# Kernel tuning notes

Measured on AMD Instinct MI355X. Metric: run time of the kernel, lower is better.

Reference implementation:

```python
import jax, jax.numpy as jnp
import numpy as np

TEMPERATURE = 0.07
EPS = 1e-8  # torch CosineSimilarity eps


def setup_inputs() -> dict:
    key = jax.random.key(0)
    k1, k2, k3 = jax.random.split(key, 3)
    N, D = 8192, 512
    features = jax.random.normal(k1, (N, D), dtype=jnp.float32)
    positive_mask = jax.random.randint(k2, (N, N), 0, 2, dtype=jnp.int32)
    negative_mask = jax.random.randint(k3, (N, N), 0, 2, dtype=jnp.int32)
    return {"features": features, "positive_mask": positive_mask, "negative_mask": negative_mask}


def reference(features, positive_mask, negative_mask):
    N = positive_mask.shape[0]
    self_contrast = 1.0 - jnp.eye(N, dtype=features.dtype)  # zero diagonal
    pos = positive_mask.astype(features.dtype) * self_contrast  # [N, N]
    neg = negative_mask.astype(features.dtype) * self_contrast  # [N, N]

    # cosine similarity via normalized matmul (same math as broadcasted CosineSimilarity)
    norm = jnp.maximum(jnp.linalg.norm(features, axis=1, keepdims=True), EPS)
    fn = features / norm  # [N, D]
    sim = jnp.matmul(fn, fn.T) / TEMPERATURE  # [N, N]

    logits_max = jax.lax.stop_gradient(jnp.max(sim, axis=1, keepdims=True))
    e = jnp.exp(sim - logits_max)  # [N, N]

    positives = e * pos
    log_neg_sum = jnp.log(jnp.sum(e * neg, axis=1, keepdims=True))  # [N, 1]
    log_prob = positives - log_neg_sum  # [N, N] (faithful to source: exp-masked, not log)

    cardinal = jnp.sum(pos, axis=1)
    cardinal = jnp.where(cardinal == 0, 1.0, cardinal)
    log_prob_sum = jnp.sum(log_prob * pos, axis=1)
    loss = -log_prob_sum / cardinal
    return jnp.mean(loss)
```

## Files before the change

kernel.cpp:

```cpp
#include <hip/hip_runtime.h>
#include <hip/hip_bf16.h>
#include <math.h>

#define NN 8192
#define DD 512
#define INV_T 14.285714285714286f

typedef __attribute__((ext_vector_type(8))) short s16x8;
typedef __attribute__((ext_vector_type(4))) float f32x4;

__device__ __forceinline__ unsigned short f32_to_bf16(float f) {
  unsigned int u = __float_as_uint(f);
  u += 0x7FFFu + ((u >> 16) & 1u);
  return (unsigned short)(u >> 16);
}

__device__ __forceinline__ void async16(const void* g, void* l) {
  __builtin_amdgcn_global_load_lds((__attribute__((address_space(1))) void*)(void*)g,
                                   (__attribute__((address_space(3))) void*)l,
                                   16, 0, 0);
}

__global__ __launch_bounds__(256) void normalize_kernel(const float* __restrict__ f,
                                                        unsigned short* __restrict__ fnb,
                                                        float* __restrict__ acc) {
  if (blockIdx.x < 96) acc[blockIdx.x * 256 + threadIdx.x] = 0.f;

  const int wave = threadIdx.x >> 6;
  const int lane = threadIdx.x & 63;
  const int row  = blockIdx.x * 4 + wave;
  const float* src = f + (size_t)row * DD + lane * 8;
  float4 v0 = *(const float4*)src;
  float4 v1 = *(const float4*)(src + 4);
  float ss = v0.x*v0.x + v0.y*v0.y + v0.z*v0.z + v0.w*v0.w
           + v1.x*v1.x + v1.y*v1.y + v1.z*v1.z + v1.w*v1.w;
  #pragma unroll
  for (int o = 32; o; o >>= 1) ss += __shfl_xor(ss, o);
  const float r = 1.0f / fmaxf(sqrtf(ss), 1e-8f);
  ushort4 a, b;
  a.x = f32_to_bf16(v0.x * r); a.y = f32_to_bf16(v0.y * r);
  a.z = f32_to_bf16(v0.z * r); a.w = f32_to_bf16(v0.w * r);
  b.x = f32_to_bf16(v1.x * r); b.y = f32_to_bf16(v1.y * r);
  b.z = f32_to_bf16(v1.z * r); b.w = f32_to_bf16(v1.w * r);
  unsigned short* dst = fnb + (size_t)row * DD + lane * 8;
  *(ushort4*)dst = a;
  *(ushort4*)(dst + 4) = b;
}

__global__ __launch_bounds__(256, 3) void fused_kernel(const unsigned short* __restrict__ fnb,
                                                       const int* __restrict__ posm,
                                                       const int* __restrict__ negm,
                                                       float* __restrict__ Spos,
                                                       float* __restrict__ Sneg,
                                                       float* __restrict__ Pcnt) {
  const int bid = blockIdx.x;
  int bi = (int)(64.5 - sqrt(64.5 * 64.5 - 2.0 * (double)bid));
  while (64 * bi - bi * (bi - 1) / 2 > bid) --bi;
  while (64 * (bi + 1) - (bi + 1) * bi / 2 <= bid) ++bi;
  const int bj = bi + (bid - (64 * bi - bi * (bi - 1) / 2));
  const int I = bi * 128;
  const int J = bj * 128;
  const bool offdiag = (bi != bj);

  const int tid  = threadIdx.x;
  const int wave = tid >> 6;
  const int lane = tid & 63;
  const int wm = wave >> 1;
  const int wn = wave & 1;
  const int q   = lane >> 4;
  const int c16 = lane & 15;

  __shared__ alignas(16) unsigned short lA[128 * 32];
  __shared__ alignas(16) unsigned short lB[128 * 32];
  __shared__ float sacc[2][128][3];
  __shared__ unsigned long long pk[4][128][2];
  for (int t = tid; t < 2 * 128 * 3; t += 256) ((float*)sacc)[t] = 0.f;

  f32x4 acc[4][4];
  const f32x4 z4 = {0.f, 0.f, 0.f, 0.f};
  #pragma unroll
  for (int mt = 0; mt < 4; ++mt)
    #pragma unroll
    for (int nt = 0; nt < 4; ++nt) acc[mt][nt] = z4;

  for (int kk = 0; kk < DD / 32; ++kk) {
    const int k0 = kk * 32;
    #pragma unroll
    for (int c = 0; c < 2; ++c) {
      const int fidx = tid + c * 256;
      const int L    = fidx >> 2;
      const int p    = fidx & 3;
      const int csrc = (p ^ ((L >> 1) & 3)) & 3;
      async16(fnb + (size_t)(I + L) * DD + k0 + csrc * 8, (char*)lA + fidx * 16);
      const int gB = 4 * (L & 31) + (L >> 5);
      async16(fnb + (size_t)(J + gB) * DD + k0 + csrc * 8, (char*)lB + fidx * 16);
    }
    __syncthreads();

    const int kd    = kk & 3;
    const int slice = kk >> 2;
    const bool mact = (kd < 2) || offdiag;
    int mv[16];
    if (mact) {
      const int rbase = (kd & 2) ? J : I;
      const int cbase = (kd & 2) ? I : J;
      const int* __restrict__ mp = (kd & 1) ? negm : posm;
      const int trow0 = slice * 32 + wave * 8;
      #pragma unroll
      for (int j = 0; j < 16; ++j) {
        const int trow = trow0 + (j >> 1);
        mv[j] = mp[(size_t)(rbase + trow) * NN + cbase + (j & 1) * 64 + lane];
      }
    }

    s16x8 aF[4], bF[4];
    #pragma unroll
    for (int t = 0; t < 4; ++t) {
      const int arow = wm * 64 + t * 16 + c16;
      const int apos = (q ^ ((arow >> 1) & 3)) & 3;
      aF[t] = *(const s16x8*)((const char*)lA + arow * 64 + apos * 16);
      const int Lb = (wn * 16 + c16) | (t << 5);
      const int bpos = (q ^ ((Lb >> 1) & 3)) & 3;
      bF[t] = *(const s16x8*)((const char*)lB + Lb * 64 + bpos * 16);
    }
    #pragma unroll
    for (int mt = 0; mt < 4; ++mt)
      #pragma unroll
      for (int nt = 0; nt < 4; ++nt)
        acc[mt][nt] = __builtin_amdgcn_mfma_f32_16x16x32_bf16(aF[mt], bF[nt], acc[mt][nt], 0, 0, 0);

    if (mact) {
      const int trow0 = slice * 32 + wave * 8;
      #pragma unroll
      for (int j = 0; j < 16; ++j) {
        const unsigned long long b = __ballot(mv[j] != 0);
        if (lane == j) pk[kd][trow0 + (j >> 1)][j & 1] = b;
      }
    }
    __syncthreads();
  }

  #pragma unroll
  for (int mt = 0; mt < 4; ++mt)
    #pragma unroll
    for (int nt = 0; nt < 4; ++nt)
      #pragma unroll
      for (int r = 0; r < 4; ++r)
        acc[mt][nt][r] = __expf(acc[mt][nt][r] * INV_T - INV_T);

  const bool hasdiag = (bi == bj) && (wm == wn);
  const int cb = wn * 64 + 4 * c16;
  const int half = c16 >> 3;
  const int bsh  = 4 * (c16 & 7);

  #pragma unroll
  for (int mt = 0; mt < 4; ++mt) {
    const int rl = wm * 64 + mt * 16 + q * 4;
    #pragma unroll
    for (int r = 0; r < 4; ++r) {
      const int row = rl + r;
      const uint2 pw = *(const uint2*)&pk[0][row][wn];
      const uint2 nw = *(const uint2*)&pk[1][row][wn];
      const unsigned int p32 = half ? pw.y : pw.x;
      const unsigned int n32 = half ? nw.y : nw.x;
      float dsp = 0.f, dsn = 0.f, dpc = 0.f;
      #pragma unroll
      for (int nt = 0; nt < 4; ++nt) {
        float pf = (float)((p32 >> (bsh + nt)) & 1u);
        float nf = (float)((n32 >> (bsh + nt)) & 1u);
        if (hasdiag && (row == cb + nt)) { pf = 0.f; nf = 0.f; }
        const float e = acc[mt][nt][r];
        dsp = fmaf(e, pf, dsp);
        dsn = fmaf(e, nf, dsn);
        dpc += pf;
      }
      #pragma unroll
      for (int o = 1; o <= 8; o <<= 1) {
        dsp += __shfl_xor(dsp, o);
        dsn += __shfl_xor(dsn, o);
        dpc += __shfl_xor(dpc, o);
      }
      if (c16 == 0) {
        atomicAdd(&sacc[0][row][0], dsp);
        atomicAdd(&sacc[0][row][1], dsn);
        atomicAdd(&sacc[0][row][2], dpc);
      }
    }
  }

  if (offdiag) {
    #pragma unroll
    for (int nt = 0; nt < 4; ++nt) {
      const int trl = cb + nt;
      const uint2 pw = *(const uint2*)&pk[2][trl][wm];
      const uint2 nw = *(const uint2*)&pk[3][trl][wm];
      float ts = 0.f, tn = 0.f, tp = 0.f;
      #pragma unroll
      for (int mt = 0; mt < 4; ++mt) {
        const unsigned int p32 = (mt < 2) ? pw.x : pw.y;
        const unsigned int n32 = (mt < 2) ? nw.x : nw.y;
        #pragma unroll
        for (int r = 0; r < 4; ++r) {
          const int bit = (mt & 1) * 16 + q * 4 + r;
          const float pf = (float)((p32 >> bit) & 1u);
          const float nf = (float)((n32 >> bit) & 1u);
          const float e = acc[mt][nt][r];
          ts = fmaf(e, pf, ts);
          tn = fmaf(e, nf, tn);
          tp += pf;
        }
      }
      ts += __shfl_xor(ts, 16); ts += __shfl_xor(ts, 32);
      tn += __shfl_xor(tn, 16); tn += __shfl_xor(tn, 32);
      tp += __shfl_xor(tp, 16); tp += __shfl_xor(tp, 32);
      if (q == 0) {
        atomicAdd(&sacc[1][trl][0], ts);
        atomicAdd(&sacc[1][trl][1], tn);
        atomicAdd(&sacc[1][trl][2], tp);
      }
    }
  }

  __syncthreads();

  const int r = tid & 127;
  if (tid < 128) {
    atomicAdd(&Spos[I + r], sacc[0][r][0]);
    atomicAdd(&Sneg[I + r], sacc[0][r][1]);
    atomicAdd(&Pcnt[I + r], sacc[0][r][2]);
  } else if (offdiag) {
    atomicAdd(&Spos[J + r], sacc[1][r][0]);
    atomicAdd(&Sneg[J + r], sacc[1][r][1]);
    atomicAdd(&Pcnt[J + r], sacc[1][r][2]);
  }
}

__global__ __launch_bounds__(256) void finalize_kernel(const float* __restrict__ Spos,
                                                       const float* __restrict__ Sneg,
                                                       const float* __restrict__ Pcnt,
                                                       float* __restrict__ out) {
  float local = 0.f;
  for (int i = threadIdx.x; i < NN; i += 256) {
    const float sp = Spos[i], sn = Sneg[i], pc = Pcnt[i];
    const float card = (pc == 0.f) ? 1.f : pc;
    local += (logf(sn) * pc - sp) / card;
  }
  #pragma unroll
  for (int o = 32; o; o >>= 1) local += __shfl_xor(local, o);
  __shared__ float red[4];
  if ((threadIdx.x & 63) == 0) red[threadIdx.x >> 6] = local;
  __syncthreads();
  if (threadIdx.x == 0)
    out[0] = (red[0] + red[1] + red[2] + red[3]) * (1.0f / (float)NN);
}

extern "C" void kernel_launch(void* const* d_in, const int* in_sizes, int n_in,
                              void* d_out, int out_size, void* d_ws, size_t ws_size,
                              hipStream_t stream) {
  const float* feat = (const float*)d_in[0];
  const int* posm   = (const int*)d_in[1];
  const int* negm   = (const int*)d_in[2];
  float* out = (float*)d_out;

  char* ws = (char*)d_ws;
  unsigned short* fnb = (unsigned short*)ws;
  float* Spos = (float*)(ws + (size_t)8 * 1024 * 1024);
  float* Sneg = Spos + NN;
  float* Pcnt = Sneg + NN;

  normalize_kernel<<<NN / 4, 256, 0, stream>>>(feat, fnb, Spos);
  fused_kernel<<<2080, 256, 0, stream>>>(fnb, posm, negm, Spos, Sneg, Pcnt);
  finalize_kernel<<<1, 256, 0, stream>>>(Spos, Sneg, Pcnt, out);
}
```

Before: 568.6 us.

## Pre-pack int masks into bitmasks in prep kernel, load bits in fused kernel

Mask bit-packing moves out of the GEMM main loop into the normalization kernel, which streams both int32 masks once with nontemporal loads and writes 64-bit ballot words to workspace. The fused kernel then loads the packed words for its tile pair into shared memory up front, so its K loop no longer issues scattered int32 mask loads that compete with the MFMA work. In exchange the prep kernel now carries the full mask read, and there is an extra write and read of the small packed arrays. The pk shared array is padded to avoid bank conflicts.

```diff
diff --git a/kernel.cpp b/kernel.cpp
--- a/kernel.cpp
+++ b/kernel.cpp
@@ -21,14 +21,19 @@
                                    16, 0, 0);
 }
 
-__global__ __launch_bounds__(256) void normalize_kernel(const float* __restrict__ f,
-                                                        unsigned short* __restrict__ fnb,
-                                                        float* __restrict__ acc) {
+__global__ __launch_bounds__(256) void prep_kernel(const float* __restrict__ f,
+                                                   const int* __restrict__ posm,
+                                                   const int* __restrict__ negm,
+                                                   unsigned short* __restrict__ fnb,
+                                                   unsigned long long* __restrict__ pkp,
+                                                   unsigned long long* __restrict__ pkn,
+                                                   float* __restrict__ acc) {
   if (blockIdx.x < 96) acc[blockIdx.x * 256 + threadIdx.x] = 0.f;
 
   const int wave = threadIdx.x >> 6;
   const int lane = threadIdx.x & 63;
   const int row  = blockIdx.x * 4 + wave;
+
   const float* src = f + (size_t)row * DD + lane * 8;
   float4 v0 = *(const float4*)src;
   float4 v1 = *(const float4*)(src + 4);
@@ -45,11 +50,35 @@
   unsigned short* dst = fnb + (size_t)row * DD + lane * 8;
   *(ushort4*)dst = a;
   *(ushort4*)(dst + 4) = b;
+
+  const int* __restrict__ prow = posm + (size_t)row * NN;
+  const int* __restrict__ nrow = negm + (size_t)row * NN;
+  #pragma unroll 2
+  for (int w = 0; w < 128; w += 4) {
+    unsigned long long pb[4], nb[4];
+    int pv[4], nv[4];
+    #pragma unroll
+    for (int u = 0; u < 4; ++u) {
+      pv[u] = __builtin_nontemporal_load(prow + (w + u) * 64 + lane);
+      nv[u] = __builtin_nontemporal_load(nrow + (w + u) * 64 + lane);
+    }
+    #pragma unroll
+    for (int u = 0; u < 4; ++u) {
+      pb[u] = __ballot(pv[u] != 0);
+      nb[u] = __ballot(nv[u] != 0);
+    }
+    unsigned long long rp = pb[0], rn = nb[0];
+    rp = ((lane & 3) == 1) ? pb[1] : rp;  rn = ((lane & 3) == 1) ? nb[1] : rn;
+    rp = ((lane & 3) == 2) ? pb[2] : rp;  rn = ((lane & 3) == 2) ? nb[2] : rn;
+    rp = ((lane & 3) == 3) ? pb[3] : rp;  rn = ((lane & 3) == 3) ? nb[3] : rn;
+    if (lane < 4)               pkp[(size_t)row * 128 + w + lane]       = rp;
+    else if (lane < 8)          pkn[(size_t)row * 128 + w + (lane - 4)] = rn;
+  }
 }
 
 __global__ __launch_bounds__(256, 3) void fused_kernel(const unsigned short* __restrict__ fnb,
-                                                       const int* __restrict__ posm,
-                                                       const int* __restrict__ negm,
+                                                       const unsigned long long* __restrict__ pkp,
+                                                       const unsigned long long* __restrict__ pkn,
                                                        float* __restrict__ Spos,
                                                        float* __restrict__ Sneg,
                                                        float* __restrict__ Pcnt) {
@@ -73,8 +102,21 @@
   __shared__ alignas(16) unsigned short lA[128 * 32];
   __shared__ alignas(16) unsigned short lB[128 * 32];
   __shared__ float sacc[2][128][3];
-  __shared__ unsigned long long pk[4][128][2];
+  __shared__ unsigned long long pk[4][128][3];
   for (int t = tid; t < 2 * 128 * 3; t += 256) ((float*)sacc)[t] = 0.f;
+
+  #pragma unroll
+  for (int p = 0; p < 2; ++p) {
+    const int idx  = tid + p * 256;
+    const int kind = idx >> 7;
+    const int row  = idx & 127;
+    const int rb   = (kind & 2) ? J : I;
+    const int cb6  = (kind & 2) ? (I >> 6) : (J >> 6);
+    const unsigned long long* __restrict__ m = (kind & 1) ? pkn : pkp;
+    const ulonglong2 v = *(const ulonglong2*)(m + (size_t)(rb + row) * 128 + cb6);
+    pk[kind][row][0] = v.x;
+    pk[kind][row][1] = v.y;
+  }
 
   f32x4 acc[4][4];
   const f32x4 z4 = {0.f, 0.f, 0.f, 0.f};
@@ -97,22 +139,6 @@
     }
     __syncthreads();
 
-    const int kd    = kk & 3;
-    const int slice = kk >> 2;
-    const bool mact = (kd < 2) || offdiag;
-    int mv[16];
-    if (mact) {
-      const int rbase = (kd & 2) ? J : I;
-      const int cbase = (kd & 2) ? I : J;
-      const int* __restrict__ mp = (kd & 1) ? negm : posm;
-      const int trow0 = slice * 32 + wave * 8;
-      #pragma unroll
-      for (int j = 0; j < 16; ++j) {
-        const int trow = trow0 + (j >> 1);
-        mv[j] = mp[(size_t)(rbase + trow) * NN + cbase + (j & 1) * 64 + lane];
-      }
-    }
-
     s16x8 aF[4], bF[4];
     #pragma unroll
     for (int t = 0; t < 4; ++t) {
@@ -128,15 +154,6 @@
       #pragma unroll
       for (int nt = 0; nt < 4; ++nt)
         acc[mt][nt] = __builtin_amdgcn_mfma_f32_16x16x32_bf16(aF[mt], bF[nt], acc[mt][nt], 0, 0, 0);
-
-    if (mact) {
-      const int trow0 = slice * 32 + wave * 8;
-      #pragma unroll
-      for (int j = 0; j < 16; ++j) {
-        const unsigned long long b = __ballot(mv[j] != 0);
-        if (lane == j) pk[kd][trow0 + (j >> 1)][j & 1] = b;
-      }
-    }
     __syncthreads();
   }
 
@@ -263,12 +280,14 @@
   float* out = (float*)d_out;
 
   char* ws = (char*)d_ws;
-  unsigned short* fnb = (unsigned short*)ws;
-  float* Spos = (float*)(ws + (size_t)8 * 1024 * 1024);
+  unsigned short* fnb      = (unsigned short*)ws;
+  unsigned long long* pkp  = (unsigned long long*)(ws + (size_t) 8*1024*1024);
+  unsigned long long* pkn  = (unsigned long long*)(ws + (size_t)16*1024*1024);
+  float* Spos = (float*)(ws + (size_t)24 * 1024 * 1024);
   float* Sneg = Spos + NN;
   float* Pcnt = Sneg + NN;
 
-  normalize_kernel<<<NN / 4, 256, 0, stream>>>(feat, fnb, Spos);
-  fused_kernel<<<2080, 256, 0, stream>>>(fnb, posm, negm, Spos, Sneg, Pcnt);
+  prep_kernel<<<NN / 4, 256, 0, stream>>>(feat, posm, negm, fnb, pkp, pkn, Spos);
+  fused_kernel<<<2080, 256, 0, stream>>>(fnb, pkp, pkn, Spos, Sneg, Pcnt);
   finalize_kernel<<<1, 256, 0, stream>>>(Spos, Sneg, Pcnt, out);
 }
```

After: 613.4 us. 1.08x slower.
